# Optimization experiments

Measured on AMD Instinct MI355X. Metric: run time of the kernel, lower is better.

Reference implementation:

```python
import jax, jax.numpy as jnp
import numpy as np


def setup_inputs() -> dict:
    key = jax.random.key(0)
    B, H, N = 1024, 8, 64
    A = jax.random.normal(key, (B, H, N, N), dtype=jnp.float32)
    # Build SPD matrices: P = A A^T / N + eps * I (eigenvalues strictly > 0)
    P = jnp.einsum('bhij,bhkj->bhik', A, A) / N + 1e-3 * jnp.eye(N, dtype=jnp.float32)
    return {"P": P}


def reference(P):
    # LogEig: eigendecompose each SPD matrix, take log of eigenvalues,
    # reconstruct X = U diag(log w) U^T  (batched over [B, H]).
    w, U = jnp.linalg.eigh(P)          # w: [B,H,N], U: [B,H,N,N]
    logw = jnp.log(w)
    return jnp.einsum('bhik,bhk,bhjk->bhij', U, logw, U)
```

## Files before the change

### kernel.cpp

```cpp
#include <hip/hip_runtime.h>
#include <math.h>

#define N 64
#define LDC 68
#define MAX_SWEEPS 10
#define SKIP_TOL2 9e-12f

__device__ __forceinline__ float frcp(float x)   { return __builtin_amdgcn_rcpf(x); }
__device__ __forceinline__ float fsqrt_(float x) { return __builtin_amdgcn_sqrtf(x); }
__device__ __forceinline__ float frsq(float x)   { return __builtin_amdgcn_rsqf(x); }
__device__ __forceinline__ float flog_(float x)  { return __builtin_amdgcn_logf(x) * 0.69314718056f; }

template <int CTRL>
__device__ __forceinline__ float dpp_add(float x) {
    int m = __builtin_amdgcn_update_dpp(0, __float_as_int(x), CTRL, 0xF, 0xF, true);
    return x + __int_as_float(m);
}

__global__ __launch_bounds__(256)
void logeig_kernel(const float* __restrict__ P, float* __restrict__ Out) {
    __shared__ float As[N * LDC];
    __shared__ float nrm[N];
    __shared__ float lw[N];
    __shared__ int ncv[2];

    const int t = threadIdx.x;
    const int bid = blockIdx.x;
    const float* A0 = P + (size_t)bid * (N * N);
    float* O = Out + (size_t)bid * (N * N);

    {
        const float4* A4 = (const float4*)A0;
        #pragma unroll
        for (int kk = 0; kk < 4; ++kk) {
            int f = t + kk * 256;
            float4 v = A4[f];
            int e = f << 2;
            int r = e >> 6;
            int i = e & 63;
            *(float4*)&As[r * LDC + i] = v;
        }
    }
    __syncthreads();

    for (int k = 0; k < N; ++k) {
        float dval = fmaxf(As[k * LDC + k], 1e-20f);
        float dinv = frsq(dval);
        for (int i = k + 1 + t; i < N; i += 256) As[k * LDC + i] *= dinv;
        if (t == 0) As[k * LDC + k] = dval * dinv;
        __syncthreads();
        for (int j = k + 1 + (t >> 3); j < N; j += 32) {
            float ljk = As[k * LDC + j];
            for (int i = j + (t & 7); i < N; i += 8)
                As[j * LDC + i] = fmaf(-As[k * LDC + i], ljk, As[j * LDC + i]);
        }
        __syncthreads();
    }

    for (int f = t; f < N * N; f += 256) {
        int c = f >> 6, i = f & 63;
        if (i < c) As[c * LDC + i] = 0.f;
    }
    if (t == 0) { ncv[0] = 0; ncv[1] = 0; }
    __syncthreads();
    if (t < N) {
        float s = 0.f;
        const float* cc = &As[t * LDC];
        for (int i = 0; i < N; ++i) { float x = cc[i]; s = fmaf(x, x, s); }
        nrm[t] = s;
    }
    __syncthreads();

    const int kp = t >> 3;
    const int g  = t & 7;
    float* colg = As + 4 * g;

    int p, q;
    if (kp == 0) { p = 63; q = 0; } else { p = kp; q = 63 - kp; }
    unsigned rotated = 0;
    int conv = 0;

    for (int sweep = 0; sweep < MAX_SWEEPS && !conv; ++sweep) {
        for (int r = 0; r < 63; ++r) {
            float* cp = colg + p * LDC;
            float* cq = colg + q * LDC;
            float4 ap0 = *(float4*)cp;
            float4 ap1 = *(float4*)(cp + 32);
            float4 aq0 = *(float4*)cq;
            float4 aq1 = *(float4*)(cq + 32);
            float a = nrm[p], b = nrm[q];
            float gd = ap0.x * aq0.x;
            gd = fmaf(ap0.y, aq0.y, gd);
            gd = fmaf(ap0.z, aq0.z, gd);
            gd = fmaf(ap0.w, aq0.w, gd);
            gd = fmaf(ap1.x, aq1.x, gd);
            gd = fmaf(ap1.y, aq1.y, gd);
            gd = fmaf(ap1.z, aq1.z, gd);
            gd = fmaf(ap1.w, aq1.w, gd);
            gd = dpp_add<0xB1>(gd);
            gd = dpp_add<0x4E>(gd);
            gd = dpp_add<0x141>(gd);
            if (gd * gd > SKIP_TOL2 * a * b) {
                float tau = (b - a) * 0.5f * frcp(gd);
                float tt = frcp(fabsf(tau) + fsqrt_(fmaf(tau, tau, 1.f)));
                if (tau < 0.f) tt = -tt;
                float c = frsq(fmaf(tt, tt, 1.f));
                float s = tt * c;
                float4 np0, np1, nq0, nq1;
                np0.x = c * ap0.x - s * aq0.x;  nq0.x = s * ap0.x + c * aq0.x;
                np0.y = c * ap0.y - s * aq0.y;  nq0.y = s * ap0.y + c * aq0.y;
                np0.z = c * ap0.z - s * aq0.z;  nq0.z = s * ap0.z + c * aq0.z;
                np0.w = c * ap0.w - s * aq0.w;  nq0.w = s * ap0.w + c * aq0.w;
                np1.x = c * ap1.x - s * aq1.x;  nq1.x = s * ap1.x + c * aq1.x;
                np1.y = c * ap1.y - s * aq1.y;  nq1.y = s * ap1.y + c * aq1.y;
                np1.z = c * ap1.z - s * aq1.z;  nq1.z = s * ap1.z + c * aq1.z;
                np1.w = c * ap1.w - s * aq1.w;  nq1.w = s * ap1.w + c * aq1.w;
                *(float4*)cp = np0;
                *(float4*)(cp + 32) = np1;
                *(float4*)cq = nq0;
                *(float4*)(cq + 32) = nq1;
                if (g == 0) {
                    nrm[p] = a - tt * gd;
                    nrm[q] = b + tt * gd;
                }
                rotated = 1;
            }
            __syncthreads();
            q = (q == 62) ? 0 : q + 1;
            if (kp) p = (p == 62) ? 0 : p + 1;
        }
        if (rotated) ncv[sweep & 1] = 1;
        if (t == 0) ncv[(sweep & 1) ^ 1] = 0;
        rotated = 0;
        __syncthreads();
        conv = (ncv[sweep & 1] == 0);
    }

    if (t < N) {
        float s = 0.f;
        const float* cc = &As[t * LDC];
        for (int i = 0; i < N; ++i) { float x = cc[i]; s = fmaf(x, x, s); }
        s = fmaxf(s, 1e-30f);
        lw[t] = flog_(s) * frcp(s);
    }
    __syncthreads();

    {
        int ti = t >> 4;
        int tj = t & 15;
        float acc[4][4];
        #pragma unroll
        for (int a2 = 0; a2 < 4; ++a2)
            #pragma unroll
            for (int b2 = 0; b2 < 4; ++b2) acc[a2][b2] = 0.f;

        for (int k = 0; k < N; ++k) {
            float w = lw[k];
            float4 ui = *(const float4*)&As[k * LDC + 4 * ti];
            float4 uj = *(const float4*)&As[k * LDC + 4 * tj];
            uj.x *= w; uj.y *= w; uj.z *= w; uj.w *= w;
            float ua[4] = {ui.x, ui.y, ui.z, ui.w};
            float ub[4] = {uj.x, uj.y, uj.z, uj.w};
            #pragma unroll
            for (int a2 = 0; a2 < 4; ++a2)
                #pragma unroll
                for (int b2 = 0; b2 < 4; ++b2)
                    acc[a2][b2] = fmaf(ua[a2], ub[b2], acc[a2][b2]);
        }
        #pragma unroll
        for (int a2 = 0; a2 < 4; ++a2) {
            float4 vout = make_float4(acc[a2][0], acc[a2][1], acc[a2][2], acc[a2][3]);
            ((float4*)O)[(4 * ti + a2) * 16 + tj] = vout;
        }
    }
}

extern "C" void kernel_launch(void* const* d_in, const int* in_sizes, int n_in,
                              void* d_out, int out_size, void* d_ws, size_t ws_size,
                              hipStream_t stream) {
    const float* P = (const float*)d_in[0];
    float* Out = (float*)d_out;
    int nmat = in_sizes[0] / (N * N);
    logeig_kernel<<<dim3(nmat), dim3(256), 0, stream>>>(P, Out);
}
```

Measured before the change: 3.033 ms.

## Run one-sided Jacobi per matrix in a single wavefront with register-resident columns

Each block shrinks to one 64-lane wavefront. Every lane keeps one column of the Cholesky factor in registers and gets its Jacobi partner column through ds_bpermute, so the per-round __syncthreads and LDS column traffic go away. Convergence is checked with a wave-level __any instead of shared flags. The cost is a 64-float partner copy per lane each round, heavy register use that may spill, and fewer threads for the Cholesky and output GEMM phases.

```diff
diff --git a/kernel.cpp b/kernel.cpp
--- a/kernel.cpp
+++ b/kernel.cpp
@@ -11,18 +11,14 @@
 __device__ __forceinline__ float frsq(float x)   { return __builtin_amdgcn_rsqf(x); }
 __device__ __forceinline__ float flog_(float x)  { return __builtin_amdgcn_logf(x) * 0.69314718056f; }
 
-template <int CTRL>
-__device__ __forceinline__ float dpp_add(float x) {
-    int m = __builtin_amdgcn_update_dpp(0, __float_as_int(x), CTRL, 0xF, 0xF, true);
-    return x + __int_as_float(m);
+__device__ __forceinline__ float bperm(int idx, float v) {
+    return __int_as_float(__builtin_amdgcn_ds_bpermute(idx, __float_as_int(v)));
 }
 
-__global__ __launch_bounds__(256)
+__global__ __launch_bounds__(64, 2)
 void logeig_kernel(const float* __restrict__ P, float* __restrict__ Out) {
     __shared__ float As[N * LDC];
-    __shared__ float nrm[N];
-    __shared__ float lw[N];
-    __shared__ int ncv[2];
+    __shared__ float lw_s[N];
 
     const int t = threadIdx.x;
     const int bid = blockIdx.x;
@@ -32,8 +28,8 @@
     {
         const float4* A4 = (const float4*)A0;
         #pragma unroll
-        for (int kk = 0; kk < 4; ++kk) {
-            int f = t + kk * 256;
+        for (int kk = 0; kk < 16; ++kk) {
+            int f = kk * 64 + t;
             float4 v = A4[f];
             int e = f << 2;
             int r = e >> 6;
@@ -46,10 +42,13 @@
     for (int k = 0; k < N; ++k) {
         float dval = fmaxf(As[k * LDC + k], 1e-20f);
         float dinv = frsq(dval);
-        for (int i = k + 1 + t; i < N; i += 256) As[k * LDC + i] *= dinv;
+        {
+            int i = k + 1 + t;
+            if (i < N) As[k * LDC + i] *= dinv;
+        }
         if (t == 0) As[k * LDC + k] = dval * dinv;
         __syncthreads();
-        for (int j = k + 1 + (t >> 3); j < N; j += 32) {
+        for (int j = k + 1 + (t >> 3); j < N; j += 8) {
             float ljk = As[k * LDC + j];
             for (int i = j + (t & 7); i < N; i += 8)
                 As[j * LDC + i] = fmaf(-As[k * LDC + i], ljk, As[j * LDC + i]);
@@ -57,120 +56,137 @@
         __syncthreads();
     }
 
-    for (int f = t; f < N * N; f += 256) {
-        int c = f >> 6, i = f & 63;
-        if (i < c) As[c * LDC + i] = 0.f;
-    }
-    if (t == 0) { ncv[0] = 0; ncv[1] = 0; }
+    for (int f = t; f < N * N; f += 64) {
+        int cc = f >> 6, i = f & 63;
+        if (i < cc) As[cc * LDC + i] = 0.f;
+    }
     __syncthreads();
-    if (t < N) {
-        float s = 0.f;
-        const float* cc = &As[t * LDC];
-        for (int i = 0; i < N; ++i) { float x = cc[i]; s = fmaf(x, x, s); }
-        nrm[t] = s;
-    }
-    __syncthreads();
-
-    const int kp = t >> 3;
-    const int g  = t & 7;
-    float* colg = As + 4 * g;
-
-    int p, q;
-    if (kp == 0) { p = 63; q = 0; } else { p = kp; q = 63 - kp; }
-    unsigned rotated = 0;
+
+    float own[N];
+    #pragma unroll
+    for (int i4 = 0; i4 < 16; ++i4) {
+        float4 v = *(const float4*)&As[t * LDC + 4 * i4];
+        own[4 * i4 + 0] = v.x;
+        own[4 * i4 + 1] = v.y;
+        own[4 * i4 + 2] = v.z;
+        own[4 * i4 + 3] = v.w;
+    }
+    float nrm;
+    {
+        float d0 = 0.f, d1 = 0.f, d2 = 0.f, d3 = 0.f;
+        #pragma unroll
+        for (int i = 0; i < N; i += 4) {
+            d0 = fmaf(own[i + 0], own[i + 0], d0);
+            d1 = fmaf(own[i + 1], own[i + 1], d1);
+            d2 = fmaf(own[i + 2], own[i + 2], d2);
+            d3 = fmaf(own[i + 3], own[i + 3], d3);
+        }
+        nrm = (d0 + d1) + (d2 + d3);
+    }
+
     int conv = 0;
-
+    #pragma unroll 1
     for (int sweep = 0; sweep < MAX_SWEEPS && !conv; ++sweep) {
+        int rot = 0;
+        #pragma unroll 1
         for (int r = 0; r < 63; ++r) {
-            float* cp = colg + p * LDC;
-            float* cq = colg + q * LDC;
-            float4 ap0 = *(float4*)cp;
-            float4 ap1 = *(float4*)(cp + 32);
-            float4 aq0 = *(float4*)cq;
-            float4 aq1 = *(float4*)(cq + 32);
-            float a = nrm[p], b = nrm[q];
-            float gd = ap0.x * aq0.x;
-            gd = fmaf(ap0.y, aq0.y, gd);
-            gd = fmaf(ap0.z, aq0.z, gd);
-            gd = fmaf(ap0.w, aq0.w, gd);
-            gd = fmaf(ap1.x, aq1.x, gd);
-            gd = fmaf(ap1.y, aq1.y, gd);
-            gd = fmaf(ap1.z, aq1.z, gd);
-            gd = fmaf(ap1.w, aq1.w, gd);
-            gd = dpp_add<0xB1>(gd);
-            gd = dpp_add<0x4E>(gd);
-            gd = dpp_add<0x141>(gd);
+            int pl;
+            bool top;
+            if (t == 63)     { pl = r;  top = true;  }
+            else if (t == r) { pl = 63; top = false; }
+            else {
+                pl = 2 * r - t;
+                if (pl < 0) pl += 63; else if (pl >= 63) pl -= 63;
+                int d = t - r; if (d < 0) d += 63;
+                top = (d <= 31);
+            }
+            int idx = pl << 2;
+            float bn = bperm(idx, nrm);
+            float prt[N];
+            #pragma unroll
+            for (int i = 0; i < N; ++i) prt[i] = bperm(idx, own[i]);
+            float d0 = 0.f, d1 = 0.f, d2 = 0.f, d3 = 0.f;
+            #pragma unroll
+            for (int i = 0; i < N; i += 4) {
+                d0 = fmaf(own[i + 0], prt[i + 0], d0);
+                d1 = fmaf(own[i + 1], prt[i + 1], d1);
+                d2 = fmaf(own[i + 2], prt[i + 2], d2);
+                d3 = fmaf(own[i + 3], prt[i + 3], d3);
+            }
+            float gd = (d0 + d1) + (d2 + d3);
+            float a = top ? nrm : bn;
+            float b = top ? bn : nrm;
             if (gd * gd > SKIP_TOL2 * a * b) {
                 float tau = (b - a) * 0.5f * frcp(gd);
                 float tt = frcp(fabsf(tau) + fsqrt_(fmaf(tau, tau, 1.f)));
                 if (tau < 0.f) tt = -tt;
                 float c = frsq(fmaf(tt, tt, 1.f));
                 float s = tt * c;
-                float4 np0, np1, nq0, nq1;
-                np0.x = c * ap0.x - s * aq0.x;  nq0.x = s * ap0.x + c * aq0.x;
-                np0.y = c * ap0.y - s * aq0.y;  nq0.y = s * ap0.y + c * aq0.y;
-                np0.z = c * ap0.z - s * aq0.z;  nq0.z = s * ap0.z + c * aq0.z;
-                np0.w = c * ap0.w - s * aq0.w;  nq0.w = s * ap0.w + c * aq0.w;
-                np1.x = c * ap1.x - s * aq1.x;  nq1.x = s * ap1.x + c * aq1.x;
-                np1.y = c * ap1.y - s * aq1.y;  nq1.y = s * ap1.y + c * aq1.y;
-                np1.z = c * ap1.z - s * aq1.z;  nq1.z = s * ap1.z + c * aq1.z;
-                np1.w = c * ap1.w - s * aq1.w;  nq1.w = s * ap1.w + c * aq1.w;
-                *(float4*)cp = np0;
-                *(float4*)(cp + 32) = np1;
-                *(float4*)cq = nq0;
-                *(float4*)(cq + 32) = nq1;
-                if (g == 0) {
-                    nrm[p] = a - tt * gd;
-                    nrm[q] = b + tt * gd;
-                }
-                rotated = 1;
+                float sg = top ? -s : s;
+                #pragma unroll
+                for (int i = 0; i < N; ++i)
+                    own[i] = fmaf(sg, prt[i], c * own[i]);
+                float tsg = top ? -tt : tt;
+                nrm = fmaf(tsg, gd, nrm);
+                rot = 1;
             }
-            __syncthreads();
-            q = (q == 62) ? 0 : q + 1;
-            if (kp) p = (p == 62) ? 0 : p + 1;
-        }
-        if (rotated) ncv[sweep & 1] = 1;
-        if (t == 0) ncv[(sweep & 1) ^ 1] = 0;
-        rotated = 0;
-        __syncthreads();
-        conv = (ncv[sweep & 1] == 0);
-    }
-
-    if (t < N) {
-        float s = 0.f;
-        const float* cc = &As[t * LDC];
-        for (int i = 0; i < N; ++i) { float x = cc[i]; s = fmaf(x, x, s); }
-        s = fmaxf(s, 1e-30f);
-        lw[t] = flog_(s) * frcp(s);
+        }
+        conv = !__any(rot);
+    }
+
+    #pragma unroll
+    for (int i4 = 0; i4 < 16; ++i4) {
+        float4 v = make_float4(own[4 * i4 + 0], own[4 * i4 + 1],
+                               own[4 * i4 + 2], own[4 * i4 + 3]);
+        *(float4*)&As[t * LDC + 4 * i4] = v;
+    }
+    {
+        float d0 = 0.f, d1 = 0.f, d2 = 0.f, d3 = 0.f;
+        #pragma unroll
+        for (int i = 0; i < N; i += 4) {
+            d0 = fmaf(own[i + 0], own[i + 0], d0);
+            d1 = fmaf(own[i + 1], own[i + 1], d1);
+            d2 = fmaf(own[i + 2], own[i + 2], d2);
+            d3 = fmaf(own[i + 3], own[i + 3], d3);
+        }
+        float lam = fmaxf((d0 + d1) + (d2 + d3), 1e-30f);
+        lw_s[t] = flog_(lam) * frcp(lam);
     }
     __syncthreads();
 
     {
         int ti = t >> 4;
         int tj = t & 15;
-        float acc[4][4];
-        #pragma unroll
-        for (int a2 = 0; a2 < 4; ++a2)
+        float acc[16][4];
+        #pragma unroll
+        for (int a2 = 0; a2 < 16; ++a2)
             #pragma unroll
             for (int b2 = 0; b2 < 4; ++b2) acc[a2][b2] = 0.f;
 
         for (int k = 0; k < N; ++k) {
-            float w = lw[k];
-            float4 ui = *(const float4*)&As[k * LDC + 4 * ti];
-            float4 uj = *(const float4*)&As[k * LDC + 4 * tj];
-            uj.x *= w; uj.y *= w; uj.z *= w; uj.w *= w;
-            float ua[4] = {ui.x, ui.y, ui.z, ui.w};
-            float ub[4] = {uj.x, uj.y, uj.z, uj.w};
-            #pragma unroll
-            for (int a2 = 0; a2 < 4; ++a2)
+            float w = lw_s[k];
+            const float* ck = &As[k * LDC];
+            float4 ub = *(const float4*)&ck[4 * tj];
+            ub.x *= w; ub.y *= w; ub.z *= w; ub.w *= w;
+            float vb[4] = {ub.x, ub.y, ub.z, ub.w};
+            float4 ua0 = *(const float4*)&ck[16 * ti + 0];
+            float4 ua1 = *(const float4*)&ck[16 * ti + 4];
+            float4 ua2 = *(const float4*)&ck[16 * ti + 8];
+            float4 ua3 = *(const float4*)&ck[16 * ti + 12];
+            float va[16] = {ua0.x, ua0.y, ua0.z, ua0.w,
+                            ua1.x, ua1.y, ua1.z, ua1.w,
+                            ua2.x, ua2.y, ua2.z, ua2.w,
+                            ua3.x, ua3.y, ua3.z, ua3.w};
+            #pragma unroll
+            for (int a2 = 0; a2 < 16; ++a2)
                 #pragma unroll
                 for (int b2 = 0; b2 < 4; ++b2)
-                    acc[a2][b2] = fmaf(ua[a2], ub[b2], acc[a2][b2]);
-        }
-        #pragma unroll
-        for (int a2 = 0; a2 < 4; ++a2) {
+                    acc[a2][b2] = fmaf(va[a2], vb[b2], acc[a2][b2]);
+        }
+        #pragma unroll
+        for (int a2 = 0; a2 < 16; ++a2) {
             float4 vout = make_float4(acc[a2][0], acc[a2][1], acc[a2][2], acc[a2][3]);
-            ((float4*)O)[(4 * ti + a2) * 16 + tj] = vout;
+            ((float4*)O)[(16 * ti + a2) * 16 + tj] = vout;
         }
     }
 }
@@ -181,5 +197,5 @@
     const float* P = (const float*)d_in[0];
     float* Out = (float*)d_out;
     int nmat = in_sizes[0] / (N * N);
-    logeig_kernel<<<dim3(nmat), dim3(256), 0, stream>>>(P, Out);
+    logeig_kernel<<<dim3(nmat), dim3(64), 0, stream>>>(P, Out);
 }
```

Result: slower. 3.504 ms (+15.5%).
